# Kernel tuning notes

Measured on AMD Instinct MI355X. Metric: run time of the kernel, lower is better.

Reference implementation:

```python
import jax, jax.numpy as jnp
import numpy as np

D_MODEL = 1024
NUM_HEADS = 16
HEAD_DIM = D_MODEL // NUM_HEADS  # 64
ROPE_THETA = 10000.0
SEQ_LEN = 4096
BATCH = 1


def apply_rope(x, positions, theta=ROPE_THETA):
    # x: [b, h, s, d], positions: [s]
    d = x.shape[-1]
    inv_freq = theta ** (-jnp.arange(0, d, 2, dtype=jnp.float32) / d)  # [d/2]
    angles = positions.astype(jnp.float32)[:, None] * inv_freq[None, :]  # [s, d/2]
    cos = jnp.cos(angles)  # [s, d/2]
    sin = jnp.sin(angles)
    x1 = x[..., 0::2]  # [b, h, s, d/2]
    x2 = x[..., 1::2]
    r1 = x1 * cos - x2 * sin
    r2 = x1 * sin + x2 * cos
    # interleave back to [..., d]
    out = jnp.stack([r1, r2], axis=-1).reshape(x.shape)
    return out.astype(x.dtype)


def setup_inputs() -> dict:
    key = jax.random.key(0)
    k_x, k_qkv, k_o = jax.random.split(key, 3)
    scale_in = 1.0 / np.sqrt(D_MODEL)
    return {
        "x": jax.random.normal(k_x, (BATCH, SEQ_LEN, D_MODEL), dtype=jnp.float32),
        "token_positions": jnp.arange(SEQ_LEN, dtype=jnp.int64 if jax.config.jax_enable_x64 else jnp.int32),
        "w_qkv": jax.random.normal(k_qkv, (3 * D_MODEL, D_MODEL), dtype=jnp.float32) * scale_in,
        "w_o": jax.random.normal(k_o, (D_MODEL, D_MODEL), dtype=jnp.float32) * scale_in,
    }


def reference(x, token_positions, w_qkv, w_o):
    b, s, _ = x.shape
    # QKV projection (Linear without bias, weight [out, in])
    x_qkv = jnp.einsum('bsd,ed->bse', x, w_qkv)  # [b, s, 3*d_model]
    # rearrange 'b s (three heads kv) -> three b heads s kv'
    x_qkv = x_qkv.reshape(b, s, 3, NUM_HEADS, HEAD_DIM)
    x_qkv = jnp.transpose(x_qkv, (2, 0, 3, 1, 4))  # [3, b, h, s, d]
    q, k, v = x_qkv[0], x_qkv[1], x_qkv[2]
    q = apply_rope(q, token_positions)
    k = apply_rope(k, token_positions)
    # scaled dot-product attention with causal mask
    scores = jnp.einsum('bhnd,bhmd->bhnm', q, k) / jnp.sqrt(jnp.float32(HEAD_DIM))
    causal = jnp.tril(jnp.ones((s, s), dtype=bool))  # [s, s]
    scores = jnp.where(causal[None, None], scores, jnp.float32(-jnp.inf))
    weights = jax.nn.softmax(scores, axis=-1)
    attn = jnp.einsum('bhnm,bhmd->bhnd', weights, v)  # [b, h, s, d]
    attn = jnp.transpose(attn, (0, 2, 1, 3)).reshape(b, s, NUM_HEADS * HEAD_DIM)
    return jnp.einsum('bsd,ed->bse', attn, w_o)
```

## Files before the change

kernel.cpp:

```cpp
#include <hip/hip_runtime.h>

#define SEQ 4096
#define DMODEL 1024
#define HEADS 16
#define HD 64
#define NQKV 3072

typedef __attribute__((ext_vector_type(8))) __bf16 bf16x8;
typedef __attribute__((ext_vector_type(4))) __bf16 bf16x4;
typedef __attribute__((ext_vector_type(8))) short short8;
typedef __attribute__((ext_vector_type(4))) float f32x4;

__device__ __forceinline__ unsigned short f2bf(float f) {
    unsigned u = __builtin_bit_cast(unsigned, f);
    return (unsigned short)((u + 0x7fffu + ((u >> 16) & 1u)) >> 16);
}
__device__ __forceinline__ float bf2f(unsigned short h) {
    return __builtin_bit_cast(float, (unsigned)h << 16);
}

__device__ __forceinline__ void gload16(const void* g, void* l) {
    __builtin_amdgcn_global_load_lds(
        (const __attribute__((address_space(1))) unsigned int*)g,
        (__attribute__((address_space(3))) unsigned int*)l, 16, 0, 0);
}

__global__ void f2bf_all(const float* __restrict__ x, const float* __restrict__ wqkv,
                         const float* __restrict__ wo, unsigned short* __restrict__ dst) {
    const int N0 = SEQ * DMODEL / 4;
    const int N1 = N0 + NQKV * DMODEL / 4;
    const int NT = N1 + DMODEL * DMODEL / 4;
    int i = blockIdx.x * 256 + threadIdx.x;
    int stride = gridDim.x * 256;
    for (; i < NT; i += stride) {
        const float4* src;
        if (i < N0)      src = reinterpret_cast<const float4*>(x) + i;
        else if (i < N1) src = reinterpret_cast<const float4*>(wqkv) + (i - N0);
        else             src = reinterpret_cast<const float4*>(wo) + (i - N1);
        float4 f = *src;
        ushort4 o;
        o.x = f2bf(f.x); o.y = f2bf(f.y); o.z = f2bf(f.z); o.w = f2bf(f.w);
        reinterpret_cast<ushort4*>(dst)[i] = o;
    }
}

template <int EPI>
__global__ __launch_bounds__(256) void gemm_bt(const unsigned short* __restrict__ A,
                                               const unsigned short* __restrict__ B,
                                               float* __restrict__ outF,
                                               unsigned short* __restrict__ outB,
                                               int M, int N, int K) {
    alignas(16) __shared__ unsigned short a_lds[2][128 * 32];
    alignas(16) __shared__ unsigned short b_lds[2][128 * 32];
    const int tid = threadIdx.x;
    const int wave = tid >> 6, lane = tid & 63;
    const int l16 = lane & 15, g = lane >> 4;
    const int wr = wave >> 1, wc = wave & 1;
    const int bm = blockIdx.x, bn = blockIdx.y;

    const int lrow = lane >> 2;
    const int lcol = (lane & 3) * 8;

    const unsigned short* Ag = A + (size_t)(bm * 128 + lrow) * K + lcol;
    const unsigned short* Bg = B + (size_t)(bn * 128 + lrow) * K + lcol;

    f32x4 acc[4][4] = {};
    const int NS = K / 32;

    auto STAGE = [&](int b, int ks) {
#pragma unroll
        for (int j = 0; j < 2; ++j) {
            int chunk = wave * 2 + j;
            gload16(Ag + (size_t)(chunk * 16) * K + ks * 32, a_lds[b] + chunk * 512);
            gload16(Bg + (size_t)(chunk * 16) * K + ks * 32, b_lds[b] + chunk * 512);
        }
    };

    STAGE(0, 0);

    for (int ks = 0; ks < NS; ++ks) {
        const int cur = ks & 1;
        asm volatile("s_waitcnt vmcnt(0)" ::: "memory");
        __builtin_amdgcn_s_barrier();
        if (ks + 1 < NS) STAGE(cur ^ 1, ks + 1);

        bf16x8 af[4], bfr[4];
#pragma unroll
        for (int m = 0; m < 4; ++m)
            af[m] = *reinterpret_cast<const bf16x8*>(a_lds[cur] + (wr * 64 + m * 16 + l16) * 32 + g * 8);
#pragma unroll
        for (int n = 0; n < 4; ++n)
            bfr[n] = *reinterpret_cast<const bf16x8*>(b_lds[cur] + (wc * 64 + n * 16 + l16) * 32 + g * 8);
        __builtin_amdgcn_s_setprio(1);
#pragma unroll
        for (int m = 0; m < 4; ++m)
#pragma unroll
            for (int n = 0; n < 4; ++n)
                acc[m][n] = __builtin_amdgcn_mfma_f32_16x16x32_bf16(af[m], bfr[n], acc[m][n], 0, 0, 0);
        __builtin_amdgcn_s_setprio(0);
    }

#pragma unroll
    for (int m = 0; m < 4; ++m)
#pragma unroll
        for (int n = 0; n < 4; ++n)
#pragma unroll
            for (int r = 0; r < 4; ++r) {
                int row = bm * 128 + wr * 64 + m * 16 + g * 4 + r;
                int col = bn * 128 + wc * 64 + n * 16 + l16;
                float v = acc[m][n][r];
                if (EPI == 0) {
                    int part = col >> 10;
                    int hd = col & 1023;
                    int h = hd >> 6, d = hd & 63;
                    outB[(size_t)((part * HEADS + h) * SEQ + row) * HD + d] = f2bf(v);
                } else {
                    outF[(size_t)row * N + col] = v;
                }
            }
}

__global__ __launch_bounds__(256) void rope_kernel(unsigned short* qkv, const int* __restrict__ pos) {
    int idx = blockIdx.x * 256 + threadIdx.x;
    int chunk = idx & 7;
    int row = idx >> 3;
    int s = row & (SEQ - 1);
    int ph = row >> 12;
    float p = (float)pos[s];
    float scale = (ph < HEADS) ? 0.125f * 1.4426950408889634f : 1.0f;
    unsigned short* base = qkv + ((size_t)ph * SEQ + s) * HD + chunk * 8;
    short8 v = *reinterpret_cast<short8*>(base);
    short8 o;
    const float k = -13.287712379549449f / 32.0f;
#pragma unroll
    for (int j = 0; j < 4; ++j) {
        int i = chunk * 4 + j;
        float ang = p * exp2f((float)i * k);
        float sn, cs;
        sincosf(ang, &sn, &cs);
        float x1 = bf2f((unsigned short)v[2 * j]);
        float x2 = bf2f((unsigned short)v[2 * j + 1]);
        o[2 * j]     = (short)f2bf((x1 * cs - x2 * sn) * scale);
        o[2 * j + 1] = (short)f2bf((x1 * sn + x2 * cs) * scale);
    }
    *reinterpret_cast<short8*>(base) = o;
}

__global__ __launch_bounds__(256) void transpose_v(const unsigned short* __restrict__ qkv,
                                                   unsigned short* __restrict__ vt) {
    const int st = blockIdx.x;
    const int h = blockIdx.y;
    __shared__ unsigned short tile[64][72];
    const unsigned short* Vg = qkv + (size_t)((2 * HEADS + h) * SEQ) * HD;
    const int tid = threadIdx.x;
#pragma unroll
    for (int j = 0; j < 2; ++j) {
        int b = (tid + j * 256) * 8;
        int row = b >> 6;
        int col = b & 63;
        short8 v = *reinterpret_cast<const short8*>(Vg + (size_t)(st * 64 + row) * HD + col);
#pragma unroll
        for (int i = 0; i < 8; ++i) tile[row][col + i] = (unsigned short)v[i];
    }
    __syncthreads();
#pragma unroll
    for (int j = 0; j < 2; ++j) {
        int b = (tid + j * 256) * 8;
        int d = b >> 6;
        int sc = b & 63;
        short8 o;
#pragma unroll
        for (int i = 0; i < 8; ++i) o[i] = (short)tile[sc + i][d];
        *reinterpret_cast<short8*>(vt + (size_t)(h * HD + d) * SEQ + st * 64 + sc) = o;
    }
}

__global__ __launch_bounds__(512) void attn_kernel(const unsigned short* __restrict__ qkv,
                                                   const unsigned short* __restrict__ vt,
                                                   unsigned short* __restrict__ attnout) {
    const int bid = blockIdx.x;
    const int xcd = bid & 7;
    const int slt = bid >> 3;
    const int j = slt & 31, hlf = slt >> 5;
    const int h = xcd * 2 + (j & 1);
    const int qb = hlf ? (j >> 1) : (31 - (j >> 1));

    const int tid = threadIdx.x;
    const int wave = tid >> 6, lane = tid & 63;
    const int l16 = lane & 15, g = lane >> 4;

    alignas(16) __shared__ unsigned short k_lds[2][128 * 64];
    alignas(16) __shared__ unsigned short v_lds[2][2][64 * 64];
    alignas(16) __shared__ unsigned short p_lds[8][16 * 64];

    const unsigned short* Qg = qkv + (size_t)((0 * HEADS + h) * SEQ) * HD;
    const unsigned short* Kg = qkv + (size_t)((1 * HEADS + h) * SEQ) * HD;
    const unsigned short* VTg = vt + (size_t)h * HD * SEQ;

    const int qbase = qb * 128 + wave * 16;
    bf16x8 qf[2];
    qf[0] = *reinterpret_cast<const bf16x8*>(Qg + (size_t)(qbase + l16) * HD + g * 8);
    qf[1] = *reinterpret_cast<const bf16x8*>(Qg + (size_t)(qbase + l16) * HD + 32 + g * 8);

    bf16x8 ones;
#pragma unroll
    for (int j2 = 0; j2 < 8; ++j2) ones[j2] = (__bf16)1.0f;

    f32x4 o_acc[4] = {};
    f32x4 l_acc = {};
    float m_r = -1e30f;

    char* pwave = (char*)p_lds + wave * 2048;
    const int rsw = (l16 & 7) << 4;

    auto STAGE = [&](int b, int kt) {
#pragma unroll
        for (int i = 0; i < 2; ++i) {
            int base = wave * 2048 + i * 1024;
            int byte = base + lane * 16;
            int krow = byte >> 7;
            int kc8 = ((byte >> 4) & 7) ^ (krow & 7);
            gload16(Kg + (size_t)(kt * 128 + krow) * HD + kc8 * 8, (char*)k_lds[b] + base);
            int fr = byte >> 7;
            int h64 = fr >> 6, vd = fr & 63;
            int vc8 = ((byte >> 4) & 7) ^ (vd & 7);
            gload16(VTg + (size_t)vd * SEQ + kt * 128 + h64 * 64 + vc8 * 8,
                    (char*)v_lds[b] + base);
        }
    };

    STAGE(0, 0);

    for (int kt = 0; kt <= qb; ++kt) {
        const int cur = kt & 1;
        asm volatile("s_waitcnt vmcnt(0)" ::: "memory");
        __builtin_amdgcn_s_barrier();
        if (kt < qb) STAGE(cur ^ 1, kt + 1);

        const bool doB = (kt * 128 + 64) <= (qbase + 15);

        f32x4 s[8] = {};
        __builtin_amdgcn_s_setprio(1);
#pragma unroll
        for (int nt = 0; nt < 4; ++nt) {
            int row = nt * 16 + l16;
#pragma unroll
            for (int kk = 0; kk < 2; ++kk) {
                bf16x8 kf = *reinterpret_cast<const bf16x8*>(
                    (char*)k_lds[cur] + row * 128 + (((kk * 4 + g) << 4) ^ rsw));
                s[nt] = __builtin_amdgcn_mfma_f32_16x16x32_bf16(kf, qf[kk], s[nt], 0, 0, 0);
            }
        }
        if (doB) {
#pragma unroll
            for (int nt = 0; nt < 4; ++nt) {
                int row = 64 + nt * 16 + l16;
#pragma unroll
                for (int kk = 0; kk < 2; ++kk) {
                    bf16x8 kf = *reinterpret_cast<const bf16x8*>(
                        (char*)k_lds[cur] + row * 128 + (((kk * 4 + g) << 4) ^ rsw));
                    s[4 + nt] = __builtin_amdgcn_mfma_f32_16x16x32_bf16(kf, qf[kk], s[4 + nt], 0, 0, 0);
                }
            }
        }
        __builtin_amdgcn_s_setprio(0);

        if (kt * 128 + 127 > qbase) {
            int qrow = qbase + l16;
#pragma unroll
            for (int nt = 0; nt < 4; ++nt)
#pragma unroll
                for (int r = 0; r < 4; ++r) {
                    int kv = kt * 128 + nt * 16 + g * 4 + r;
                    if (kv > qrow) s[nt][r] = -1e30f;
                    if (kv + 64 > qrow) s[4 + nt][r] = -1e30f;
                }
        }

        f32x4 m4;
#pragma unroll
        for (int r = 0; r < 4; ++r) {
            float a = fmaxf(fmaxf(s[0][r], s[1][r]), fmaxf(s[2][r], s[3][r]));
            float b = fmaxf(fmaxf(s[4][r], s[5][r]), fmaxf(s[6][r], s[7][r]));
            m4[r] = fmaxf(a, b);
        }
        float mx = fmaxf(fmaxf(m4[0], m4[1]), fmaxf(m4[2], m4[3]));
        mx = fmaxf(mx, __shfl_xor(mx, 16));
        mx = fmaxf(mx, __shfl_xor(mx, 32));

        if (__any(mx > m_r + 8.0f)) {
            float mnew = fmaxf(m_r, mx);
            float alpha = __builtin_amdgcn_exp2f(m_r - mnew);
            m_r = mnew;
#pragma unroll
            for (int dt = 0; dt < 4; ++dt)
#pragma unroll
                for (int r = 0; r < 4; ++r) o_acc[dt][r] *= alpha;
            l_acc[0] *= alpha;
        }

#pragma unroll
        for (int i = 0; i < 8; ++i)
#pragma unroll
            for (int r = 0; r < 4; ++r) s[i][r] = __builtin_amdgcn_exp2f(s[i][r] - m_r);

        __builtin_amdgcn_s_setprio(1);
#pragma unroll
        for (int h64 = 0; h64 < 2; ++h64) {
            if (h64 && !doB) break;
#pragma unroll
            for (int nt = 0; nt < 4; ++nt) {
                bf16x4 pb;
#pragma unroll
                for (int r = 0; r < 4; ++r) pb[r] = (__bf16)s[h64 * 4 + nt][r];
                *reinterpret_cast<bf16x4*>(pwave + l16 * 128 + ((nt * 32 + g * 8) ^ rsw)) = pb;
            }
            bf16x8 pfrag[2];
#pragma unroll
            for (int kk = 0; kk < 2; ++kk)
                pfrag[kk] = *reinterpret_cast<const bf16x8*>(
                    pwave + l16 * 128 + (((kk * 4 + g) << 4) ^ rsw));

#pragma unroll
            for (int dt = 0; dt < 4; ++dt) {
                int row = dt * 16 + l16;
#pragma unroll
                for (int kk = 0; kk < 2; ++kk) {
                    bf16x8 vf = *reinterpret_cast<const bf16x8*>(
                        (char*)v_lds[cur][h64] + row * 128 + (((kk * 4 + g) << 4) ^ rsw));
                    o_acc[dt] = __builtin_amdgcn_mfma_f32_16x16x32_bf16(vf, pfrag[kk], o_acc[dt], 0, 0, 0);
                }
            }
            l_acc = __builtin_amdgcn_mfma_f32_16x16x32_bf16(ones, pfrag[0], l_acc, 0, 0, 0);
            l_acc = __builtin_amdgcn_mfma_f32_16x16x32_bf16(ones, pfrag[1], l_acc, 0, 0, 0);
        }
        __builtin_amdgcn_s_setprio(0);
    }

    float inv = 1.0f / l_acc[0];
    int q = qbase + l16;
#pragma unroll
    for (int dt = 0; dt < 4; ++dt) {
        ushort4 ov;
        ov.x = f2bf(o_acc[dt][0] * inv);
        ov.y = f2bf(o_acc[dt][1] * inv);
        ov.z = f2bf(o_acc[dt][2] * inv);
        ov.w = f2bf(o_acc[dt][3] * inv);
        *reinterpret_cast<ushort4*>(attnout + (size_t)q * DMODEL + h * HD + dt * 16 + g * 4) = ov;
    }
}

extern "C" void kernel_launch(void* const* d_in, const int* in_sizes, int n_in,
                              void* d_out, int out_size, void* d_ws, size_t ws_size,
                              hipStream_t stream) {
    const float* x = (const float*)d_in[0];
    const int* pos = (const int*)d_in[1];
    const float* wqkv = (const float*)d_in[2];
    const float* wo = (const float*)d_in[3];
    float* out = (float*)d_out;

    unsigned short* xb = (unsigned short*)d_ws;
    unsigned short* wqkvb = xb + (size_t)SEQ * DMODEL;
    unsigned short* wob = wqkvb + (size_t)NQKV * DMODEL;
    unsigned short* qkvp = wob + (size_t)DMODEL * DMODEL;
    unsigned short* vt = qkvp + (size_t)3 * HEADS * SEQ * HD;
    unsigned short* attnb = vt + (size_t)HEADS * HD * SEQ;

    f2bf_all<<<2048, 256, 0, stream>>>(x, wqkv, wo, xb);

    dim3 g1(SEQ / 128, NQKV / 128);
    gemm_bt<0><<<g1, 256, 0, stream>>>(xb, wqkvb, nullptr, qkvp, SEQ, NQKV, DMODEL);

    rope_kernel<<<(2 * HEADS * SEQ * 8) / 256, 256, 0, stream>>>(qkvp, pos);
    transpose_v<<<dim3(SEQ / 64, HEADS), 256, 0, stream>>>(qkvp, vt);
    attn_kernel<<<512, 512, 0, stream>>>(qkvp, vt, attnb);

    dim3 g2(SEQ / 128, DMODEL / 128);
    gemm_bt<1><<<g2, 256, 0, stream>>>(attnb, wob, out, nullptr, SEQ, DMODEL, DMODEL);
}
```

Baseline: 150.9 us.

## Split long causal query tiles across KV halves with persistent atomic scheduler and merge

After: 166.2 us. 10.2% more time.

```diff
diff --git a/kernel.cpp b/kernel.cpp
--- a/kernel.cpp
+++ b/kernel.cpp
@@ -177,14 +177,11 @@
 
 __global__ __launch_bounds__(512) void attn_kernel(const unsigned short* __restrict__ qkv,
                                                    const unsigned short* __restrict__ vt,
-                                                   unsigned short* __restrict__ attnout) {
-    const int bid = blockIdx.x;
-    const int xcd = bid & 7;
-    const int slt = bid >> 3;
-    const int j = slt & 31, hlf = slt >> 5;
-    const int h = xcd * 2 + (j & 1);
-    const int qb = hlf ? (j >> 1) : (31 - (j >> 1));
-
+                                                   unsigned short* __restrict__ attnout,
+                                                   int* __restrict__ qcnt,
+                                                   unsigned short* __restrict__ pO,
+                                                   float* __restrict__ lmf) {
+    const int xcd = blockIdx.x & 7;
     const int tid = threadIdx.x;
     const int wave = tid >> 6, lane = tid & 63;
     const int l16 = lane & 15, g = lane >> 4;
@@ -192,162 +189,243 @@
     alignas(16) __shared__ unsigned short k_lds[2][128 * 64];
     alignas(16) __shared__ unsigned short v_lds[2][2][64 * 64];
     alignas(16) __shared__ unsigned short p_lds[8][16 * 64];
-
-    const unsigned short* Qg = qkv + (size_t)((0 * HEADS + h) * SEQ) * HD;
-    const unsigned short* Kg = qkv + (size_t)((1 * HEADS + h) * SEQ) * HD;
-    const unsigned short* VTg = vt + (size_t)h * HD * SEQ;
-
-    const int qbase = qb * 128 + wave * 16;
-    bf16x8 qf[2];
-    qf[0] = *reinterpret_cast<const bf16x8*>(Qg + (size_t)(qbase + l16) * HD + g * 8);
-    qf[1] = *reinterpret_cast<const bf16x8*>(Qg + (size_t)(qbase + l16) * HD + 32 + g * 8);
-
-    bf16x8 ones;
-#pragma unroll
-    for (int j2 = 0; j2 < 8; ++j2) ones[j2] = (__bf16)1.0f;
-
-    f32x4 o_acc[4] = {};
-    f32x4 l_acc = {};
-    float m_r = -1e30f;
+    __shared__ int slot_sh;
 
     char* pwave = (char*)p_lds + wave * 2048;
     const int rsw = (l16 & 7) << 4;
 
-    auto STAGE = [&](int b, int kt) {
-#pragma unroll
-        for (int i = 0; i < 2; ++i) {
-            int base = wave * 2048 + i * 1024;
-            int byte = base + lane * 16;
-            int krow = byte >> 7;
-            int kc8 = ((byte >> 4) & 7) ^ (krow & 7);
-            gload16(Kg + (size_t)(kt * 128 + krow) * HD + kc8 * 8, (char*)k_lds[b] + base);
-            int fr = byte >> 7;
-            int h64 = fr >> 6, vd = fr & 63;
-            int vc8 = ((byte >> 4) & 7) ^ (vd & 7);
-            gload16(VTg + (size_t)vd * SEQ + kt * 128 + h64 * 64 + vc8 * 8,
-                    (char*)v_lds[b] + base);
+    for (;;) {
+        if (tid == 0) slot_sh = atomicAdd(&qcnt[xcd], 1);
+        __syncthreads();
+        const int t = slot_sh;
+        __syncthreads();
+        if (t >= 108) break;
+
+        int qtile, hloc, khalf, k0, k1;
+        bool isSplit;
+        if (t < 88) {
+            qtile = 31 - (t >> 2);
+            hloc = (t >> 1) & 1;
+            khalf = t & 1;
+            int T = qtile + 1, H = (T + 1) >> 1;
+            k0 = khalf ? H : 0;
+            k1 = khalf ? T : H;
+            isSplit = true;
+        } else {
+            int rem = t - 88;
+            qtile = 9 - (rem >> 1);
+            hloc = rem & 1;
+            khalf = 0;
+            k0 = 0; k1 = qtile + 1;
+            isSplit = false;
         }
-    };
-
-    STAGE(0, 0);
-
-    for (int kt = 0; kt <= qb; ++kt) {
-        const int cur = kt & 1;
-        asm volatile("s_waitcnt vmcnt(0)" ::: "memory");
-        __builtin_amdgcn_s_barrier();
-        if (kt < qb) STAGE(cur ^ 1, kt + 1);
-
-        const bool doB = (kt * 128 + 64) <= (qbase + 15);
-
-        f32x4 s[8] = {};
-        __builtin_amdgcn_s_setprio(1);
-#pragma unroll
-        for (int nt = 0; nt < 4; ++nt) {
-            int row = nt * 16 + l16;
-#pragma unroll
-            for (int kk = 0; kk < 2; ++kk) {
-                bf16x8 kf = *reinterpret_cast<const bf16x8*>(
-                    (char*)k_lds[cur] + row * 128 + (((kk * 4 + g) << 4) ^ rsw));
-                s[nt] = __builtin_amdgcn_mfma_f32_16x16x32_bf16(kf, qf[kk], s[nt], 0, 0, 0);
-            }
-        }
-        if (doB) {
+        const int h = xcd * 2 + hloc;
+
+        const unsigned short* Qg = qkv + (size_t)((0 * HEADS + h) * SEQ) * HD;
+        const unsigned short* Kg = qkv + (size_t)((1 * HEADS + h) * SEQ) * HD;
+        const unsigned short* VTg = vt + (size_t)h * HD * SEQ;
+
+        const int qbase = qtile * 128 + wave * 16;
+        bf16x8 qf[2];
+        qf[0] = *reinterpret_cast<const bf16x8*>(Qg + (size_t)(qbase + l16) * HD + g * 8);
+        qf[1] = *reinterpret_cast<const bf16x8*>(Qg + (size_t)(qbase + l16) * HD + 32 + g * 8);
+
+        bf16x8 ones;
+#pragma unroll
+        for (int j2 = 0; j2 < 8; ++j2) ones[j2] = (__bf16)1.0f;
+
+        f32x4 o_acc[4] = {};
+        f32x4 l_acc = {};
+        float m_r = -1e30f;
+
+        auto STAGE = [&](int b, int kt) {
+#pragma unroll
+            for (int i = 0; i < 2; ++i) {
+                int base = wave * 2048 + i * 1024;
+                int byte = base + lane * 16;
+                int krow = byte >> 7;
+                int kc8 = ((byte >> 4) & 7) ^ (krow & 7);
+                gload16(Kg + (size_t)(kt * 128 + krow) * HD + kc8 * 8, (char*)k_lds[b] + base);
+                int fr = byte >> 7;
+                int h64 = fr >> 6, vd = fr & 63;
+                int vc8 = ((byte >> 4) & 7) ^ (vd & 7);
+                gload16(VTg + (size_t)vd * SEQ + kt * 128 + h64 * 64 + vc8 * 8,
+                        (char*)v_lds[b] + base);
+            }
+        };
+
+        STAGE(0, k0);
+
+        for (int kt = k0; kt < k1; ++kt) {
+            const int cur = (kt - k0) & 1;
+            asm volatile("s_waitcnt vmcnt(0)" ::: "memory");
+            __builtin_amdgcn_s_barrier();
+            if (kt + 1 < k1) STAGE(cur ^ 1, kt + 1);
+
+            const bool doB = (kt * 128 + 64) <= (qbase + 15);
+
+            f32x4 s[8] = {};
+            __builtin_amdgcn_s_setprio(1);
 #pragma unroll
             for (int nt = 0; nt < 4; ++nt) {
-                int row = 64 + nt * 16 + l16;
+                int row = nt * 16 + l16;
 #pragma unroll
                 for (int kk = 0; kk < 2; ++kk) {
                     bf16x8 kf = *reinterpret_cast<const bf16x8*>(
                         (char*)k_lds[cur] + row * 128 + (((kk * 4 + g) << 4) ^ rsw));
-                    s[4 + nt] = __builtin_amdgcn_mfma_f32_16x16x32_bf16(kf, qf[kk], s[4 + nt], 0, 0, 0);
+                    s[nt] = __builtin_amdgcn_mfma_f32_16x16x32_bf16(kf, qf[kk], s[nt], 0, 0, 0);
                 }
             }
+            if (doB) {
+#pragma unroll
+                for (int nt = 0; nt < 4; ++nt) {
+                    int row = 64 + nt * 16 + l16;
+#pragma unroll
+                    for (int kk = 0; kk < 2; ++kk) {
+                        bf16x8 kf = *reinterpret_cast<const bf16x8*>(
+                            (char*)k_lds[cur] + row * 128 + (((kk * 4 + g) << 4) ^ rsw));
+                        s[4 + nt] = __builtin_amdgcn_mfma_f32_16x16x32_bf16(kf, qf[kk], s[4 + nt], 0, 0, 0);
+                    }
+                }
+            }
+            __builtin_amdgcn_s_setprio(0);
+
+            if (kt * 128 + 127 > qbase) {
+                int qrow = qbase + l16;
+#pragma unroll
+                for (int nt = 0; nt < 4; ++nt)
+#pragma unroll
+                    for (int r = 0; r < 4; ++r) {
+                        int kv = kt * 128 + nt * 16 + g * 4 + r;
+                        if (kv > qrow) s[nt][r] = -1e30f;
+                        if (kv + 64 > qrow) s[4 + nt][r] = -1e30f;
+                    }
+            }
+
+            f32x4 m4;
+#pragma unroll
+            for (int r = 0; r < 4; ++r) {
+                float a = fmaxf(fmaxf(s[0][r], s[1][r]), fmaxf(s[2][r], s[3][r]));
+                float b = fmaxf(fmaxf(s[4][r], s[5][r]), fmaxf(s[6][r], s[7][r]));
+                m4[r] = fmaxf(a, b);
+            }
+            float mx = fmaxf(fmaxf(m4[0], m4[1]), fmaxf(m4[2], m4[3]));
+            mx = fmaxf(mx, __shfl_xor(mx, 16));
+            mx = fmaxf(mx, __shfl_xor(mx, 32));
+
+            if (__any(mx > m_r + 8.0f)) {
+                float mnew = fmaxf(m_r, mx);
+                float alpha = __builtin_amdgcn_exp2f(m_r - mnew);
+                m_r = mnew;
+#pragma unroll
+                for (int dt = 0; dt < 4; ++dt)
+#pragma unroll
+                    for (int r = 0; r < 4; ++r) o_acc[dt][r] *= alpha;
+                l_acc[0] *= alpha;
+            }
+
+#pragma unroll
+            for (int i = 0; i < 8; ++i)
+#pragma unroll
+                for (int r = 0; r < 4; ++r) s[i][r] = __builtin_amdgcn_exp2f(s[i][r] - m_r);
+
+            __builtin_amdgcn_s_setprio(1);
+#pragma unroll
+            for (int h64 = 0; h64 < 2; ++h64) {
+                if (h64 && !doB) break;
+#pragma unroll
+                for (int nt = 0; nt < 4; ++nt) {
+                    bf16x4 pb;
+#pragma unroll
+                    for (int r = 0; r < 4; ++r) pb[r] = (__bf16)s[h64 * 4 + nt][r];
+                    *reinterpret_cast<bf16x4*>(pwave + l16 * 128 + ((nt * 32 + g * 8) ^ rsw)) = pb;
+                }
+                bf16x8 pfrag[2];
+#pragma unroll
+                for (int kk = 0; kk < 2; ++kk)
+                    pfrag[kk] = *reinterpret_cast<const bf16x8*>(
+                        pwave + l16 * 128 + (((kk * 4 + g) << 4) ^ rsw));
+
+#pragma unroll
+                for (int dt = 0; dt < 4; ++dt) {
+                    int row = dt * 16 + l16;
+#pragma unroll
+                    for (int kk = 0; kk < 2; ++kk) {
+                        bf16x8 vf = *reinterpret_cast<const bf16x8*>(
+                            (char*)v_lds[cur][h64] + row * 128 + (((kk * 4 + g) << 4) ^ rsw));
+                        o_acc[dt] = __builtin_amdgcn_mfma_f32_16x16x32_bf16(vf, pfrag[kk], o_acc[dt], 0, 0, 0);
+                    }
+                }
+                l_acc = __builtin_amdgcn_mfma_f32_16x16x32_bf16(ones, pfrag[0], l_acc, 0, 0, 0);
+                l_acc = __builtin_amdgcn_mfma_f32_16x16x32_bf16(ones, pfrag[1], l_acc, 0, 0, 0);
+            }
+            __builtin_amdgcn_s_setprio(0);
         }
-        __builtin_amdgcn_s_setprio(0);
-
-        if (kt * 128 + 127 > qbase) {
-            int qrow = qbase + l16;
-#pragma unroll
-            for (int nt = 0; nt < 4; ++nt)
-#pragma unroll
-                for (int r = 0; r < 4; ++r) {
-                    int kv = kt * 128 + nt * 16 + g * 4 + r;
-                    if (kv > qrow) s[nt][r] = -1e30f;
-                    if (kv + 64 > qrow) s[4 + nt][r] = -1e30f;
-                }
+
+        const int ql = wave * 16 + l16;
+        if (isSplit) {
+            int sidx = (h * 22 + (qtile - 10)) * 2 + khalf;
+            unsigned short* Op = pO + (size_t)sidx * 8192;
+#pragma unroll
+            for (int dt = 0; dt < 4; ++dt) {
+                ushort4 ov;
+                ov.x = f2bf(o_acc[dt][0]);
+                ov.y = f2bf(o_acc[dt][1]);
+                ov.z = f2bf(o_acc[dt][2]);
+                ov.w = f2bf(o_acc[dt][3]);
+                *reinterpret_cast<ushort4*>(Op + ql * 64 + dt * 16 + g * 4) = ov;
+            }
+            if (g == 0) {
+                lmf[sidx * 256 + ql] = l_acc[0];
+                lmf[sidx * 256 + 128 + ql] = m_r;
+            }
+        } else {
+            float inv = 1.0f / l_acc[0];
+            int q = qtile * 128 + ql;
+#pragma unroll
+            for (int dt = 0; dt < 4; ++dt) {
+                ushort4 ov;
+                ov.x = f2bf(o_acc[dt][0] * inv);
+                ov.y = f2bf(o_acc[dt][1] * inv);
+                ov.z = f2bf(o_acc[dt][2] * inv);
+                ov.w = f2bf(o_acc[dt][3] * inv);
+                *reinterpret_cast<ushort4*>(attnout + (size_t)q * DMODEL + h * HD + dt * 16 + g * 4) = ov;
+            }
         }
-
-        f32x4 m4;
-#pragma unroll
-        for (int r = 0; r < 4; ++r) {
-            float a = fmaxf(fmaxf(s[0][r], s[1][r]), fmaxf(s[2][r], s[3][r]));
-            float b = fmaxf(fmaxf(s[4][r], s[5][r]), fmaxf(s[6][r], s[7][r]));
-            m4[r] = fmaxf(a, b);
-        }
-        float mx = fmaxf(fmaxf(m4[0], m4[1]), fmaxf(m4[2], m4[3]));
-        mx = fmaxf(mx, __shfl_xor(mx, 16));
-        mx = fmaxf(mx, __shfl_xor(mx, 32));
-
-        if (__any(mx > m_r + 8.0f)) {
-            float mnew = fmaxf(m_r, mx);
-            float alpha = __builtin_amdgcn_exp2f(m_r - mnew);
-            m_r = mnew;
-#pragma unroll
-            for (int dt = 0; dt < 4; ++dt)
-#pragma unroll
-                for (int r = 0; r < 4; ++r) o_acc[dt][r] *= alpha;
-            l_acc[0] *= alpha;
-        }
-
-#pragma unroll
-        for (int i = 0; i < 8; ++i)
-#pragma unroll
-            for (int r = 0; r < 4; ++r) s[i][r] = __builtin_amdgcn_exp2f(s[i][r] - m_r);
-
-        __builtin_amdgcn_s_setprio(1);
-#pragma unroll
-        for (int h64 = 0; h64 < 2; ++h64) {
-            if (h64 && !doB) break;
-#pragma unroll
-            for (int nt = 0; nt < 4; ++nt) {
-                bf16x4 pb;
-#pragma unroll
-                for (int r = 0; r < 4; ++r) pb[r] = (__bf16)s[h64 * 4 + nt][r];
-                *reinterpret_cast<bf16x4*>(pwave + l16 * 128 + ((nt * 32 + g * 8) ^ rsw)) = pb;
-            }
-            bf16x8 pfrag[2];
-#pragma unroll
-            for (int kk = 0; kk < 2; ++kk)
-                pfrag[kk] = *reinterpret_cast<const bf16x8*>(
-                    pwave + l16 * 128 + (((kk * 4 + g) << 4) ^ rsw));
-
-#pragma unroll
-            for (int dt = 0; dt < 4; ++dt) {
-                int row = dt * 16 + l16;
-#pragma unroll
-                for (int kk = 0; kk < 2; ++kk) {
-                    bf16x8 vf = *reinterpret_cast<const bf16x8*>(
-                        (char*)v_lds[cur][h64] + row * 128 + (((kk * 4 + g) << 4) ^ rsw));
-                    o_acc[dt] = __builtin_amdgcn_mfma_f32_16x16x32_bf16(vf, pfrag[kk], o_acc[dt], 0, 0, 0);
-                }
-            }
-            l_acc = __builtin_amdgcn_mfma_f32_16x16x32_bf16(ones, pfrag[0], l_acc, 0, 0, 0);
-            l_acc = __builtin_amdgcn_mfma_f32_16x16x32_bf16(ones, pfrag[1], l_acc, 0, 0, 0);
-        }
-        __builtin_amdgcn_s_setprio(0);
-    }
-
-    float inv = 1.0f / l_acc[0];
-    int q = qbase + l16;
-#pragma unroll
-    for (int dt = 0; dt < 4; ++dt) {
-        ushort4 ov;
-        ov.x = f2bf(o_acc[dt][0] * inv);
-        ov.y = f2bf(o_acc[dt][1] * inv);
-        ov.z = f2bf(o_acc[dt][2] * inv);
-        ov.w = f2bf(o_acc[dt][3] * inv);
-        *reinterpret_cast<ushort4*>(attnout + (size_t)q * DMODEL + h * HD + dt * 16 + g * 4) = ov;
-    }
+    }
+}
+
+__global__ __launch_bounds__(256) void merge_kernel(const unsigned short* __restrict__ pO,
+                                                    const float* __restrict__ lmf,
+                                                    unsigned short* __restrict__ attnout) {
+    int idx = blockIdx.x * 256 + threadIdx.x;
+    if (idx >= 16 * 22 * 1024) return;
+    int h = idx / (22 * 1024);
+    int r = idx % (22 * 1024);
+    int qt = r >> 10;
+    int rr = r & 1023;
+    int q = rr >> 3, d8 = rr & 7;
+
+    int s0 = (h * 22 + qt) * 2;
+    float l0 = lmf[s0 * 256 + q],       m0 = lmf[s0 * 256 + 128 + q];
+    float l1 = lmf[(s0 + 1) * 256 + q], m1 = lmf[(s0 + 1) * 256 + 128 + q];
+    float m = fmaxf(m0, m1);
+    float a0 = __builtin_amdgcn_exp2f(m0 - m), a1 = __builtin_amdgcn_exp2f(m1 - m);
+    float L = l0 * a0 + l1 * a1;
+    float c0 = a0 / L, c1 = a1 / L;
+
+    const unsigned short* O0 = pO + (size_t)s0 * 8192 + q * 64 + d8 * 8;
+    const unsigned short* O1 = O0 + 8192;
+    short8 v0 = *reinterpret_cast<const short8*>(O0);
+    short8 v1 = *reinterpret_cast<const short8*>(O1);
+    short8 o;
+#pragma unroll
+    for (int j = 0; j < 8; ++j) {
+        float val = bf2f((unsigned short)v0[j]) * c0 + bf2f((unsigned short)v1[j]) * c1;
+        o[j] = (short)f2bf(val);
+    }
+    int qtile = qt + 10;
+    *reinterpret_cast<short8*>(attnout + (size_t)(qtile * 128 + q) * DMODEL + h * HD + d8 * 8) = o;
 }
 
 extern "C" void kernel_launch(void* const* d_in, const int* in_sizes, int n_in,
@@ -366,6 +444,11 @@
     unsigned short* vt = qkvp + (size_t)3 * HEADS * SEQ * HD;
     unsigned short* attnb = vt + (size_t)HEADS * HD * SEQ;
 
+    char* sbase = (char*)d_ws;
+    int* qcnt = (int*)sbase;
+    float* lmf = (float*)(sbase + 256);
+    unsigned short* pO = (unsigned short*)(sbase + 256 + (1 << 20));
+
     f2bf_all<<<2048, 256, 0, stream>>>(x, wqkv, wo, xb);
 
     dim3 g1(SEQ / 128, NQKV / 128);
@@ -373,7 +456,10 @@
 
     rope_kernel<<<(2 * HEADS * SEQ * 8) / 256, 256, 0, stream>>>(qkvp, pos);
     transpose_v<<<dim3(SEQ / 64, HEADS), 256, 0, stream>>>(qkvp, vt);
-    attn_kernel<<<512, 512, 0, stream>>>(qkvp, vt, attnb);
+
+    hipMemsetAsync(qcnt, 0, 64, stream);
+    attn_kernel<<<512, 512, 0, stream>>>(qkvp, vt, attnb, qcnt, pO, lmf);
+    merge_kernel<<<(16 * 22 * 1024 + 255) / 256, 256, 0, stream>>>(pO, lmf, attnb);
 
     dim3 g2(SEQ / 128, DMODEL / 128);
     gemm_bt<1><<<g2, 256, 0, stream>>>(attnb, wob, out, nullptr, SEQ, DMODEL, DMODEL);
```
